# Kernel optimization log

Measured on AMD Instinct MI355X. Metric: run time of the kernel, lower is better.

The kernel has to match this reference:

```python
import jax, jax.numpy as jnp
import numpy as np

# DenseCRF hyperparameters (match init_kwargs)
NUM_CLASS = 21
H, W = 96, 96
APP_W, SMO_W = 10.0, 3.0          # appearance_weight, smoothness_weight
PROX_STD, COLOR_STD, SMOOTH_STD = 30.0, 0.1, 3.0
ITERS = 5


def setup_inputs() -> dict:
    key = jax.random.key(0)
    k1, k2 = jax.random.split(key)
    x = jax.random.uniform(k1, (3, H, W), dtype=jnp.float32)        # RGB image in [0,1]
    yhat = jax.random.normal(k2, (NUM_CLASS, H, W), dtype=jnp.float32)  # logits
    # Potts-model incompatibility matrix: ones - eye
    mu = jnp.ones((NUM_CLASS, NUM_CLASS), jnp.float32) - jnp.eye(NUM_CLASS, dtype=jnp.float32)
    return {"x": x, "yhat": yhat, "mu": mu}


def _gauss_kernel(feats):
    """Exact Gaussian kernel K_ij = exp(-||f_i - f_j||^2 / 2), feats: (N, D).
    This is the math the permutohedral lattice splat/blur/slice approximates."""
    sq = jnp.sum(feats * feats, axis=1)                 # (N,)
    d2 = sq[:, None] + sq[None, :] - 2.0 * feats @ feats.T  # (N, N)
    return jnp.exp(-0.5 * jnp.maximum(d2, 0.0))


def reference(x, yhat, mu):
    C, Hh, Ww = yhat.shape
    # pixel coordinate grid, (2, H, W)
    yy, xx = jnp.mgrid[0:Hh, 0:Ww]
    pos = jnp.stack([yy, xx]).astype(jnp.float32)
    # bilateral features: (y, x, r, g, b) scaled by per-dim sigmas -> (N, 5)
    sig_bi = jnp.array([PROX_STD, PROX_STD, COLOR_STD, COLOR_STD, COLOR_STD], jnp.float32)
    f_bi = jnp.concatenate([pos, x], axis=0).reshape(5, -1).T / sig_bi
    # smoothness features: (y, x) / smoothness_std -> (N, 2)
    f_sm = pos.reshape(2, -1).T / SMOOTH_STD
    # "fit": build the filtering kernels once
    K_bi = _gauss_kernel(f_bi)   # (N, N)
    K_sm = _gauss_kernel(f_sm)   # (N, N)

    unary = yhat.reshape(C, -1)                 # (C, N)
    out = jax.nn.softmax(unary, axis=0)
    for _ in range(ITERS):
        app = K_bi @ out.T                      # (N, C) bilateral message passing
        smo = K_sm @ out.T                      # (N, C) spatial message passing
        pw = APP_W * app + SMO_W * smo          # (N, C)
        # einsum('ij,bi->bj', mu, pw).T  ==  (pw @ mu).T
        pw = (pw @ mu).T                        # (C, N) compatibility transform
        unary = unary + pw
        out = jax.nn.softmax(unary, axis=0)
    return out.reshape(C, Hh, Ww)
```

## Files before the change

### kernel.cpp

```cpp
#include <hip/hip_runtime.h>
#include <math.h>


#define NN 9216
#define CC 21
#define HH 96
#define WW 96
#define CP 24
#define JS2 12
#define NJ2 (NN / JS2)
#define TJ2 128
#define OST2 136

typedef _Float16 half8 __attribute__((ext_vector_type(8)));
typedef __fp16 fp16x2 __attribute__((ext_vector_type(2)));
typedef float f32x4 __attribute__((ext_vector_type(4)));

union HU { int i[4]; half8 h; };

__global__ __launch_bounds__(256) void featinit_kernel(const float* __restrict__ x,
                                                       const float* __restrict__ yhat,
                                                       float* __restrict__ feat,
                                                       float* __restrict__ unary,
                                                       _Float16* __restrict__ out_hi,
                                                       _Float16* __restrict__ out_lo,
                                                       float* __restrict__ out_cn) {
    int n = blockIdx.x * 256 + threadIdx.x;
    {
        int y = n / WW, xx = n - y * WW;
        const float inv_sqrt_ln2 = 1.2011224087864498f;
        float sp = inv_sqrt_ln2 / 30.0f;
        float sc = inv_sqrt_ln2 * 10.0f;
        float fy = (float)y * sp;
        float fx = (float)xx * sp;
        float fr = x[0 * NN + n] * sc;
        float fg = x[1 * NN + n] * sc;
        float fb = x[2 * NN + n] * sc;
        float S = fy * fy + fx * fx + fr * fr + fg * fg + fb * fb;
        float4* f4 = (float4*)(feat + (size_t)n * 8);
        f4[0] = make_float4(fy, fx, fr, fg);
        f4[1] = make_float4(fb, -0.5f * S, 0.0f, 0.0f);
    }
    float u[CC], p[CC];
    float m = -1e30f;
#pragma unroll
    for (int c = 0; c < CC; c++) { u[c] = yhat[c * NN + n]; m = fmaxf(m, u[c]); }
    float s = 0.0f;
#pragma unroll
    for (int c = 0; c < CC; c++) { p[c] = __expf(u[c] - m); s += p[c]; }
    float inv = 1.0f / s;
#pragma unroll
    for (int c = 0; c < CC; c++) p[c] *= inv;
#pragma unroll
    for (int c = 0; c < CC; c++) {
        unary[n * CP + c] = u[c];
        _Float16 ph = (_Float16)p[c];
        out_hi[(size_t)c * NN + n] = ph;
        out_lo[(size_t)c * NN + n] = (_Float16)(p[c] - (float)ph);
        out_cn[c * NN + n] = p[c];
    }
#pragma unroll
    for (int c = CC; c < CP; c++) {
        unary[n * CP + c] = 0.0f;
        out_hi[(size_t)c * NN + n] = (_Float16)0.0f;
        out_lo[(size_t)c * NN + n] = (_Float16)0.0f;
    }
}

__global__ __launch_bounds__(256, 4) void bilateral_mfma(const float* __restrict__ feat,
                                                         const _Float16* __restrict__ out_hi,
                                                         const _Float16* __restrict__ out_lo,
                                                         float* __restrict__ part) {
    __shared__ float smemf[4288];
    float* sfeat = smemf;
    _Float16* sh_ = (_Float16*)(smemf + 1024);
    _Float16* sl_ = (_Float16*)(smemf + 2656);

    const int tid = threadIdx.x;
    const int lane = tid & 63;
    const int w = tid >> 6;
    const int r = lane & 15;
    const int g = lane >> 4;
    const int i0 = blockIdx.x * 64;
    const int jslice = blockIdx.y * NJ2;

    float fi0[4], fi1[4], fi2[4], fi3[4], fi4[4], hsi[4];
#pragma unroll
    for (int m = 0; m < 4; ++m) {
        const float* fp = feat + (size_t)(i0 + m * 16 + r) * 8;
        float4 A = *(const float4*)fp;
        float2 B = *(const float2*)(fp + 4);
        fi0[m] = A.x; fi1[m] = A.y; fi2[m] = A.z; fi3[m] = A.w;
        fi4[m] = B.x; hsi[m] = B.y;
    }

    f32x4 acc[4][2];
#pragma unroll
    for (int m = 0; m < 4; ++m) { acc[m][0] = (f32x4)0.0f; acc[m][1] = (f32x4)0.0f; }

    const int jb = w * 32 + g * 8;
    const int r2 = (r < 8) ? (16 + r) : 23;

#pragma unroll 1
    for (int rd = 0; rd < NJ2 / TJ2; ++rd) {
        __syncthreads();
        {
            int j = tid >> 1, h = tid & 1;
            int jp = j ^ ((j >> 3) & 3);
            ((float4*)sfeat)[jp * 2 + h] =
                *(const float4*)(feat + (size_t)(jslice + rd * TJ2 + j) * 8 + h * 4);
        }
        for (int v = tid; v < 768; v += 256) {
            int vv = v;
            _Float16* dstbase;
            const _Float16* srcbase;
            if (vv < 384) { dstbase = sh_; srcbase = out_hi; }
            else { dstbase = sl_; srcbase = out_lo; vv -= 384; }
            int c = vv >> 4, j8 = vv & 15;
            *(float4*)(dstbase + c * OST2 + j8 * 8) =
                *(const float4*)(srcbase + (size_t)c * NN + jslice + rd * TJ2 + j8 * 8);
        }
        __syncthreads();

        int wh[4][4], wl[4][4];
#pragma unroll
        for (int tp = 0; tp < 4; ++tp) {
            const float* jp0 = sfeat + (size_t)(w * 32 + g * 8 + ((2 * tp) ^ g)) * 8;
            const float* jp1 = sfeat + (size_t)(w * 32 + g * 8 + ((2 * tp + 1) ^ g)) * 8;
            float4 A0 = *(const float4*)jp0;
            float2 B0 = *(const float2*)(jp0 + 4);
            float4 A1 = *(const float4*)jp1;
            float2 B1 = *(const float2*)(jp1 + 4);
#pragma unroll
            for (int m = 0; m < 4; ++m) {
                float d0 = hsi[m] + B0.y;
                d0 = fmaf(fi0[m], A0.x, d0);
                d0 = fmaf(fi1[m], A0.y, d0);
                d0 = fmaf(fi2[m], A0.z, d0);
                d0 = fmaf(fi3[m], A0.w, d0);
                d0 = fmaf(fi4[m], B0.x, d0);
                float d1 = hsi[m] + B1.y;
                d1 = fmaf(fi0[m], A1.x, d1);
                d1 = fmaf(fi1[m], A1.y, d1);
                d1 = fmaf(fi2[m], A1.z, d1);
                d1 = fmaf(fi3[m], A1.w, d1);
                d1 = fmaf(fi4[m], B1.x, d1);
                float k0 = __builtin_amdgcn_exp2f(d0);
                float k1 = __builtin_amdgcn_exp2f(d1);
                fp16x2 kh = __builtin_amdgcn_cvt_pkrtz(k0, k1);
                fp16x2 kl = __builtin_amdgcn_cvt_pkrtz(k0 - (float)kh.x,
                                                       k1 - (float)kh.y);
                __builtin_memcpy(&wh[m][tp], &kh, 4);
                __builtin_memcpy(&wl[m][tp], &kl, 4);
            }
        }
        half8 b0h = *(const half8*)(sh_ + r * OST2 + jb);
        half8 b0l = *(const half8*)(sl_ + r * OST2 + jb);
        half8 b1h = *(const half8*)(sh_ + r2 * OST2 + jb);
        half8 b1l = *(const half8*)(sl_ + r2 * OST2 + jb);
#pragma unroll
        for (int m = 0; m < 4; ++m) {
            HU uh, ul;
            uh.i[0] = wh[m][0]; uh.i[1] = wh[m][1];
            uh.i[2] = wh[m][2]; uh.i[3] = wh[m][3];
            ul.i[0] = wl[m][0]; ul.i[1] = wl[m][1];
            ul.i[2] = wl[m][2]; ul.i[3] = wl[m][3];
            acc[m][0] = __builtin_amdgcn_mfma_f32_16x16x32_f16(uh.h, b0h, acc[m][0], 0, 0, 0);
            acc[m][0] = __builtin_amdgcn_mfma_f32_16x16x32_f16(ul.h, b0h, acc[m][0], 0, 0, 0);
            acc[m][0] = __builtin_amdgcn_mfma_f32_16x16x32_f16(uh.h, b0l, acc[m][0], 0, 0, 0);
            acc[m][1] = __builtin_amdgcn_mfma_f32_16x16x32_f16(uh.h, b1h, acc[m][1], 0, 0, 0);
            acc[m][1] = __builtin_amdgcn_mfma_f32_16x16x32_f16(ul.h, b1h, acc[m][1], 0, 0, 0);
            acc[m][1] = __builtin_amdgcn_mfma_f32_16x16x32_f16(uh.h, b1l, acc[m][1], 0, 0, 0);
        }
    }

#pragma unroll
    for (int m = 0; m < 4; ++m) {
        __syncthreads();
        if (w != m) {
            float* dst = smemf + (size_t)(w * 64 + lane) * 12;
            *(f32x4*)(dst + 0) = acc[m][0];
            *(f32x4*)(dst + 4) = acc[m][1];
        }
        __syncthreads();
        if (w == m) {
            f32x4 s0 = acc[m][0], s1 = acc[m][1];
#pragma unroll
            for (int k = 0; k < 4; ++k) {
                if (k == m) continue;
                const float* src = smemf + (size_t)(k * 64 + lane) * 12;
                s0 += *(const f32x4*)(src + 0);
                s1 += *(const f32x4*)(src + 4);
            }
            float* pb = part + ((size_t)blockIdx.y * NN + i0 + m * 16 + g * 4) * 32 + r;
#pragma unroll
            for (int q = 0; q < 4; ++q) {
                pb[q * 32] = s0[q];
                pb[q * 32 + 16] = s1[q];
            }
        }
    }
}

__global__ __launch_bounds__(256) void smo_y_kernel(const float* __restrict__ src,
                                                    float* __restrict__ dst) {
    __shared__ float wt[2 * HH - 1];
    int tid = threadIdx.x;
    if (tid < 2 * HH - 1) {
        float d = (float)(tid - (HH - 1));
        wt[tid] = __expf(d * d * (-1.0f / 18.0f));
    }
    __syncthreads();
    int id = blockIdx.x * 256 + tid;
    int c = id / NN;
    int rem = id - c * NN;
    int y = rem / WW;
    int x = rem - y * WW;
    const float* s = src + (size_t)c * NN + x;
    float a = 0.0f;
    for (int yp = 0; yp < HH; yp++) a = fmaf(wt[yp - y + (HH - 1)], s[yp * WW], a);
    dst[id] = a;
}

__global__ __launch_bounds__(256) void smo_x_kernel(const float* __restrict__ src,
                                                    float* __restrict__ dst) {
    __shared__ float wt[2 * HH - 1];
    int tid = threadIdx.x;
    if (tid < 2 * HH - 1) {
        float d = (float)(tid - (HH - 1));
        wt[tid] = __expf(d * d * (-1.0f / 18.0f));
    }
    __syncthreads();
    int id = blockIdx.x * 256 + tid;
    int c = id / NN;
    int rem = id - c * NN;
    int y = rem / WW;
    int x = rem - y * WW;
    const float* s = src + (size_t)c * NN + y * WW;
    float a = 0.0f;
    for (int xp = 0; xp < WW; xp++) a = fmaf(wt[xp - x + (HH - 1)], s[xp], a);
    dst[id] = a;
}

__global__ __launch_bounds__(256) void combine_kernel(const float* __restrict__ part,
                                                      const float* __restrict__ smo,
                                                      const float* __restrict__ mu,
                                                      float* __restrict__ unary,
                                                      _Float16* __restrict__ out_hi,
                                                      _Float16* __restrict__ out_lo,
                                                      float* __restrict__ out_cn) {
    __shared__ float muL[CC * CC];
    __shared__ float app[256 * 33];
    int tid = threadIdx.x;
    for (int u = tid; u < CC * CC; u += 256) muL[u] = mu[u];
    const int n0 = blockIdx.x * 256;

    f32x4 a[8];
#pragma unroll
    for (int s8 = 0; s8 < 8; ++s8) a[s8] = (f32x4)0.0f;
#pragma unroll 1
    for (int k = 0; k < JS2; ++k) {
        const float* base = part + (size_t)k * NN * 32 + (size_t)n0 * 32;
#pragma unroll
        for (int s8 = 0; s8 < 8; ++s8) {
            a[s8] += *(const f32x4*)(base + (size_t)(s8 * 256 + tid) * 4);
        }
    }
#pragma unroll
    for (int s8 = 0; s8 < 8; ++s8) {
        int v = s8 * 256 + tid;
        int nl = v >> 3, c4 = v & 7;
        float* dst = app + nl * 33 + c4 * 4;
        dst[0] = a[s8][0]; dst[1] = a[s8][1]; dst[2] = a[s8][2]; dst[3] = a[s8][3];
    }
    __syncthreads();

    int n = n0 + tid;
    float pin[CC];
#pragma unroll
    for (int c = 0; c < CC; c++)
        pin[c] = 10.0f * app[tid * 33 + c] + 3.0f * smo[c * NN + n];
    float pout[CC];
#pragma unroll
    for (int j = 0; j < CC; j++) pout[j] = 0.0f;
#pragma unroll
    for (int i2 = 0; i2 < CC; i2++) {
        float v = pin[i2];
#pragma unroll
        for (int j = 0; j < CC; j++) pout[j] = fmaf(v, muL[i2 * CC + j], pout[j]);
    }
    float u[CC], p[CC];
    float m = -1e30f;
#pragma unroll
    for (int c = 0; c < CC; c++) {
        u[c] = unary[n * CP + c] + pout[c];
        m = fmaxf(m, u[c]);
    }
    float s = 0.0f;
#pragma unroll
    for (int c = 0; c < CC; c++) { p[c] = __expf(u[c] - m); s += p[c]; }
    float inv = 1.0f / s;
#pragma unroll
    for (int c = 0; c < CC; c++) p[c] *= inv;
#pragma unroll
    for (int c = 0; c < CC; c++) {
        unary[n * CP + c] = u[c];
        _Float16 ph = (_Float16)p[c];
        out_hi[(size_t)c * NN + n] = ph;
        out_lo[(size_t)c * NN + n] = (_Float16)(p[c] - (float)ph);
        out_cn[c * NN + n] = p[c];
    }
}

extern "C" void kernel_launch(void* const* d_in, const int* in_sizes, int n_in,
                              void* d_out, int out_size, void* d_ws, size_t ws_size,
                              hipStream_t stream) {
    const float* x = (const float*)d_in[0];
    const float* yhat = (const float*)d_in[1];
    const float* mu = (const float*)d_in[2];
    float* out = (float*)d_out;
    float* ws = (float*)d_ws;

    float*     feat   = ws;
    _Float16*  out_hi = (_Float16*)(ws + 73728);
    _Float16*  out_lo = (_Float16*)(ws + 184320);
    float*     unary  = ws + 294912;
    float*     smo    = ws + 516096;
    float*     tmp    = ws + 709632;
    float*     part   = ws + 903168;

    featinit_kernel<<<NN / 256, 256, 0, stream>>>(x, yhat, feat, unary, out_hi, out_lo, out);

    for (int it = 0; it < 5; it++) {
        bilateral_mfma<<<dim3(144, JS2), 256, 0, stream>>>(feat, out_hi, out_lo, part);
        smo_y_kernel<<<CC * NN / 256, 256, 0, stream>>>(out, tmp);
        smo_x_kernel<<<CC * NN / 256, 256, 0, stream>>>(tmp, smo);
        combine_kernel<<<NN / 256, 256, 0, stream>>>(part, smo, mu, unary, out_hi, out_lo, out);
    }
}
```

Measured before the change: 351.5 us.

## Fuse separable smoothness filter into bilateral MFMA launch as extra blocks

Drops the two separate smoothness-filter launches (y pass, then x pass). Their work moves into the bilateral kernel: 21 extra blocks, one per class, each run the y pass into a shared-memory plane and then the x pass from shared memory. This removes two launches per iteration plus the global temp round trip, and lets the smoothing overlap with the bilateral MFMA blocks. The trade-off is more shared memory per block, which may lower occupancy, and 21 long-running blocks that could form a tail.

```diff
diff --git a/kernel.cpp b/kernel.cpp
--- a/kernel.cpp
+++ b/kernel.cpp
@@ -11,6 +11,7 @@
 #define NJ2 (NN / JS2)
 #define TJ2 128
 #define OST2 136
+#define NBIL (144 * JS2)
 
 typedef _Float16 half8 __attribute__((ext_vector_type(8)));
 typedef __fp16 fp16x2 __attribute__((ext_vector_type(2)));
@@ -67,22 +68,58 @@
     }
 }
 
-__global__ __launch_bounds__(256, 4) void bilateral_mfma(const float* __restrict__ feat,
-                                                         const _Float16* __restrict__ out_hi,
-                                                         const _Float16* __restrict__ out_lo,
-                                                         float* __restrict__ part) {
-    __shared__ float smemf[4288];
-    float* sfeat = smemf;
-    _Float16* sh_ = (_Float16*)(smemf + 1024);
-    _Float16* sl_ = (_Float16*)(smemf + 2656);
-
+__global__ __launch_bounds__(256, 4) void bilateral_smo(const float* __restrict__ feat,
+                                                        const _Float16* __restrict__ out_hi,
+                                                        const _Float16* __restrict__ out_lo,
+                                                        float* __restrict__ part,
+                                                        const float* __restrict__ out_cn,
+                                                        float* __restrict__ smo) {
+    __shared__ float smem[9408];
     const int tid = threadIdx.x;
+    int bid = blockIdx.x;
+
+    if (bid < CC) {
+        const int c = bid;
+        float* plane = smem;
+        float* wt = smem + 9216;
+        if (tid < 2 * HH - 1) {
+            float d = (float)(tid - (HH - 1));
+            wt[tid] = __expf(d * d * (-1.0f / 18.0f));
+        }
+        __syncthreads();
+#pragma unroll 1
+        for (int k = 0; k < 36; ++k) {
+            int n = k * 256 + tid;
+            int y = n / WW, x = n - y * WW;
+            const float* s = out_cn + (size_t)c * NN + x;
+            float a = 0.0f;
+            for (int yp = 0; yp < HH; yp++) a = fmaf(wt[yp - y + (HH - 1)], s[yp * WW], a);
+            plane[n] = a;
+        }
+        __syncthreads();
+#pragma unroll 1
+        for (int k = 0; k < 36; ++k) {
+            int n = k * 256 + tid;
+            int y = n / WW, x = n - y * WW;
+            const float* s = plane + y * WW;
+            float a = 0.0f;
+            for (int xp = 0; xp < WW; xp++) a = fmaf(wt[xp - x + (HH - 1)], s[xp], a);
+            smo[(size_t)c * NN + n] = a;
+        }
+        return;
+    }
+    bid -= CC;
+
+    float* sfeat = smem;
+    _Float16* sh_ = (_Float16*)(smem + 1024);
+    _Float16* sl_ = (_Float16*)(smem + 2656);
+
     const int lane = tid & 63;
     const int w = tid >> 6;
     const int r = lane & 15;
     const int g = lane >> 4;
-    const int i0 = blockIdx.x * 64;
-    const int jslice = blockIdx.y * NJ2;
+    const int i0 = (bid % 144) * 64;
+    const int jslice = (bid / 144) * NJ2;
 
     float fi0[4], fi1[4], fi2[4], fi3[4], fi4[4], hsi[4];
 #pragma unroll
@@ -178,7 +215,7 @@
     for (int m = 0; m < 4; ++m) {
         __syncthreads();
         if (w != m) {
-            float* dst = smemf + (size_t)(w * 64 + lane) * 12;
+            float* dst = smem + (size_t)(w * 64 + lane) * 12;
             *(f32x4*)(dst + 0) = acc[m][0];
             *(f32x4*)(dst + 4) = acc[m][1];
         }
@@ -188,11 +225,11 @@
 #pragma unroll
             for (int k = 0; k < 4; ++k) {
                 if (k == m) continue;
-                const float* src = smemf + (size_t)(k * 64 + lane) * 12;
+                const float* src = smem + (size_t)(k * 64 + lane) * 12;
                 s0 += *(const f32x4*)(src + 0);
                 s1 += *(const f32x4*)(src + 4);
             }
-            float* pb = part + ((size_t)blockIdx.y * NN + i0 + m * 16 + g * 4) * 32 + r;
+            float* pb = part + ((size_t)(bid / 144) * NN + i0 + m * 16 + g * 4) * 32 + r;
 #pragma unroll
             for (int q = 0; q < 4; ++q) {
                 pb[q * 32] = s0[q];
@@ -200,46 +237,6 @@
             }
         }
     }
-}
-
-__global__ __launch_bounds__(256) void smo_y_kernel(const float* __restrict__ src,
-                                                    float* __restrict__ dst) {
-    __shared__ float wt[2 * HH - 1];
-    int tid = threadIdx.x;
-    if (tid < 2 * HH - 1) {
-        float d = (float)(tid - (HH - 1));
-        wt[tid] = __expf(d * d * (-1.0f / 18.0f));
-    }
-    __syncthreads();
-    int id = blockIdx.x * 256 + tid;
-    int c = id / NN;
-    int rem = id - c * NN;
-    int y = rem / WW;
-    int x = rem - y * WW;
-    const float* s = src + (size_t)c * NN + x;
-    float a = 0.0f;
-    for (int yp = 0; yp < HH; yp++) a = fmaf(wt[yp - y + (HH - 1)], s[yp * WW], a);
-    dst[id] = a;
-}
-
-__global__ __launch_bounds__(256) void smo_x_kernel(const float* __restrict__ src,
-                                                    float* __restrict__ dst) {
-    __shared__ float wt[2 * HH - 1];
-    int tid = threadIdx.x;
-    if (tid < 2 * HH - 1) {
-        float d = (float)(tid - (HH - 1));
-        wt[tid] = __expf(d * d * (-1.0f / 18.0f));
-    }
-    __syncthreads();
-    int id = blockIdx.x * 256 + tid;
-    int c = id / NN;
-    int rem = id - c * NN;
-    int y = rem / WW;
-    int x = rem - y * WW;
-    const float* s = src + (size_t)c * NN + y * WW;
-    float a = 0.0f;
-    for (int xp = 0; xp < WW; xp++) a = fmaf(wt[xp - x + (HH - 1)], s[xp], a);
-    dst[id] = a;
 }
 
 __global__ __launch_bounds__(256) void combine_kernel(const float* __restrict__ part,
@@ -328,13 +325,12 @@
     float*     smo    = ws + 516096;
     float*     tmp    = ws + 709632;
     float*     part   = ws + 903168;
+    (void)tmp;
 
     featinit_kernel<<<NN / 256, 256, 0, stream>>>(x, yhat, feat, unary, out_hi, out_lo, out);
 
     for (int it = 0; it < 5; it++) {
-        bilateral_mfma<<<dim3(144, JS2), 256, 0, stream>>>(feat, out_hi, out_lo, part);
-        smo_y_kernel<<<CC * NN / 256, 256, 0, stream>>>(out, tmp);
-        smo_x_kernel<<<CC * NN / 256, 256, 0, stream>>>(tmp, smo);
+        bilateral_smo<<<NBIL + CC, 256, 0, stream>>>(feat, out_hi, out_lo, part, out, smo);
         combine_kernel<<<NN / 256, 256, 0, stream>>>(part, smo, mu, unary, out_hi, out_lo, out);
     }
 }
```

New measurement: 711.7 us. 102% more time.
